# Kernel tuning notes

Measured on AMD Instinct MI355X. Metric: run time of the kernel, lower is better.

## Reference

```python
import jax, jax.numpy as jnp
import numpy as np

B, D_IN, D_CTX, UNITS, RANK = 4096, 2048, 512, 2048, 256


def setup_inputs() -> dict:
    key = jax.random.key(0)
    ks = jax.random.split(key, 6)
    scale_u = 1.0 / np.sqrt(D_IN)
    scale_w = 1.0 / np.sqrt(D_CTX)
    return {
        "inputs": jax.random.normal(ks[0], (B, D_IN), dtype=jnp.float32),
        "context": jax.random.normal(ks[1], (B, D_CTX), dtype=jnp.float32),
        "U": jax.random.normal(ks[2], (D_IN, RANK), dtype=jnp.float32) * scale_u,
        "S": jax.random.uniform(ks[3], (RANK,), dtype=jnp.float32) + 0.5,
        "V": jax.random.normal(ks[4], (UNITS, RANK), dtype=jnp.float32) * scale_u,
        "W": jax.random.normal(ks[5], (D_CTX, RANK), dtype=jnp.float32) * scale_w,
        "Bc": jnp.zeros((RANK,), dtype=jnp.float32),
        "bias": jnp.zeros((UNITS,), dtype=jnp.float32),
    }


def reference(inputs, context, U, S, V, W, Bc, bias):
    # h = context @ W + Bc ; chi = sigmoid(h) ; s[b,r] = S[r] * chi[b,r]
    chi = jax.nn.sigmoid(context @ W + Bc)           # [B, R]
    s = S * chi                                       # [B, R]
    # Original math: out[b,m] = sum_{n,r} x[b,n] U[n,r] s[b,r] V[m,r]
    # Reassociated (identical math, no [B,N,M] kernel): ((x @ U) * s) @ V^T
    proj = (inputs @ U) * s                           # [B, R]
    out = proj @ V.T + bias                           # [B, UNITS]
    return out  # activation is linear (None)
```

## Files before the change

kernel.cpp:

```cpp
#include <hip/hip_runtime.h>
#include <math.h>

namespace {

constexpr int Bdim  = 4096;
constexpr int D_IN  = 2048;
constexpr int D_CTX = 512;
constexpr int UNITS = 2048;
constexpr int RANK  = 256;
constexpr int SPLIT = 4;

typedef __bf16 bf16x8 __attribute__((ext_vector_type(8)));
typedef float  f32x4  __attribute__((ext_vector_type(4)));

__global__ __launch_bounds__(256) void k_prep(
    const float* __restrict__ U, const float* __restrict__ W,
    __bf16* __restrict__ Ut, __bf16* __restrict__ Wt) {
  const int job = blockIdx.y;
  const int t = threadIdx.x;
  const float* src = job ? W : U;
  __bf16* dst      = job ? Wt : Ut;
  const int K = job ? D_CTX : D_IN;
  const int tilesK = K / 64;
  const int tid = blockIdx.x;
  if (tid >= tilesK * 4) return;
  const int k0 = (tid % tilesK) * 64;
  const int n0 = (tid / tilesK) * 64;
  __shared__ __bf16 T[64][72];
  const int i  = t >> 4;
  const int j4 = (t & 15) * 4;
  for (int ii = i; ii < 64; ii += 16) {
    float4 v = *(const float4*)(src + (size_t)(k0 + ii) * RANK + n0 + j4);
    T[j4 + 0][ii] = (__bf16)v.x;
    T[j4 + 1][ii] = (__bf16)v.y;
    T[j4 + 2][ii] = (__bf16)v.z;
    T[j4 + 3][ii] = (__bf16)v.w;
  }
  __syncthreads();
  const int jj = t >> 3;
  const int c  = t & 7;
  for (int j2 = jj; j2 < 64; j2 += 32) {
    bf16x8 v = *(const bf16x8*)&T[j2][c * 8];
    *(bf16x8*)(dst + (size_t)(n0 + j2) * K + k0 + c * 8) = v;
  }
}

__global__ __launch_bounds__(256) void k_pg(
    const float* __restrict__ x,   const __bf16* __restrict__ Ut,
    const float* __restrict__ ctx, const __bf16* __restrict__ Wt,
    const float* __restrict__ S,   const float* __restrict__ Bc,
    __bf16* __restrict__ part, __bf16* __restrict__ s_out) {
  constexpr int BM = 64, BN = 128, BK = 64;
  __shared__ __align__(16) __bf16 As[2][BM * BK];
  __shared__ __align__(16) __bf16 Bs[2][BN * BK];
  const int t = threadIdx.x;
  const int y = blockIdx.y;
  const bool gate = (y < 2);
  const int nh    = gate ? y : ((y - 2) & 1);
  const int slice = (y - 2) >> 1;
  const int bm = blockIdx.x * BM;
  const int bn = nh * BN;
  const float*  A = gate ? ctx : x;
  const __bf16* B = gate ? Wt  : Ut;
  const int Kt   = gate ? D_CTX : D_IN;
  const int k_lo = gate ? 0 : slice * (D_IN / SPLIT);
  const int k_hi = gate ? D_CTX : k_lo + (D_IN / SPLIT);
  const int w = t >> 6, l = t & 63;
  const int wr0 = (w >> 1) * 32;
  const int wc0 = (w & 1) * 64;
  const int lrow = l & 15;
  const int lk   = l >> 4;
  f32x4 acc[2][4] = {};

  float4 a0_lo[2], a0_hi[2], a1_lo[2], a1_hi[2];
  bf16x8 b0[4], b1[4];

  auto LOADA = [&](float4 (&lo)[2], float4 (&hi)[2], int k0) {
#pragma unroll
    for (int ci = 0; ci < 2; ++ci) {
      const int c = t + ci * 256;
      const int row = c >> 3, kc = c & 7;
      const float* g = A + (size_t)(bm + row) * Kt + k0 + kc * 8;
      lo[ci] = *(const float4*)g;
      hi[ci] = *(const float4*)(g + 4);
    }
  };
  auto LOADB = [&](bf16x8 (&bb)[4], int k0) {
#pragma unroll
    for (int ci = 0; ci < 4; ++ci) {
      const int c = t + ci * 256;
      const int row = c >> 3, kc = c & 7;
      bb[ci] = *(const bf16x8*)(B + (size_t)(bn + row) * Kt + k0 + kc * 8);
    }
  };
  auto WRITEA = [&](char* dstAs, const float4 (&lo)[2], const float4 (&hi)[2]) {
#pragma unroll
    for (int ci = 0; ci < 2; ++ci) {
      const int c = t + ci * 256;
      const int row = c >> 3, kc = c & 7;
      bf16x8 v;
      v[0] = (__bf16)lo[ci].x; v[1] = (__bf16)lo[ci].y;
      v[2] = (__bf16)lo[ci].z; v[3] = (__bf16)lo[ci].w;
      v[4] = (__bf16)hi[ci].x; v[5] = (__bf16)hi[ci].y;
      v[6] = (__bf16)hi[ci].z; v[7] = (__bf16)hi[ci].w;
      *(bf16x8*)(dstAs + row * 128 + ((kc ^ (row & 7)) * 16)) = v;
    }
  };
  auto WRITEB = [&](char* dstBs, const bf16x8 (&bb)[4]) {
#pragma unroll
    for (int ci = 0; ci < 4; ++ci) {
      const int c = t + ci * 256;
      const int row = c >> 3, kc = c & 7;
      *(bf16x8*)(dstBs + row * 128 + ((kc ^ (row & 7)) * 16)) = bb[ci];
    }
  };
  auto MFMA_STEP = [&](const char* curAs, const char* curBs) {
#pragma unroll
    for (int kk = 0; kk < 2; ++kk) {
      bf16x8 af[2], bfr[4];
#pragma unroll
      for (int mf = 0; mf < 2; ++mf) {
        const int row = wr0 + mf * 16 + lrow;
        af[mf] = *(const bf16x8*)(curAs + row * 128 +
                                  (((kk * 4 + lk) ^ (row & 7)) * 16));
      }
#pragma unroll
      for (int nf = 0; nf < 4; ++nf) {
        const int row = wc0 + nf * 16 + lrow;
        bfr[nf] = *(const bf16x8*)(curBs + row * 128 +
                                   (((kk * 4 + lk) ^ (row & 7)) * 16));
      }
#pragma unroll
      for (int mf = 0; mf < 2; ++mf)
#pragma unroll
        for (int nf = 0; nf < 4; ++nf)
          acc[mf][nf] = __builtin_amdgcn_mfma_f32_16x16x32_bf16(
              af[mf], bfr[nf], acc[mf][nf], 0, 0, 0);
    }
  };

  LOADA(a0_lo, a0_hi, k_lo);
  LOADB(b0, k_lo);
  LOADA(a1_lo, a1_hi, k_lo + BK);
  LOADB(b1, k_lo + BK);
  for (int k0 = k_lo; k0 < k_hi; k0 += 2 * BK) {
    WRITEA((char*)As[0], a0_lo, a0_hi);
    WRITEB((char*)Bs[0], b0);
    __syncthreads();
    if (k0 + 2 * BK < k_hi) {
      LOADA(a0_lo, a0_hi, k0 + 2 * BK);
      LOADB(b0, k0 + 2 * BK);
    }
    MFMA_STEP((const char*)As[0], (const char*)Bs[0]);
    WRITEA((char*)As[1], a1_lo, a1_hi);
    WRITEB((char*)Bs[1], b1);
    __syncthreads();
    if (k0 + 3 * BK < k_hi) {
      LOADA(a1_lo, a1_hi, k0 + 3 * BK);
      LOADB(b1, k0 + 3 * BK);
    }
    MFMA_STEP((const char*)As[1], (const char*)Bs[1]);
  }

#pragma unroll
  for (int mf = 0; mf < 2; ++mf) {
#pragma unroll
    for (int nf = 0; nf < 4; ++nf) {
#pragma unroll
      for (int r = 0; r < 4; ++r) {
        const int m = bm + wr0 + mf * 16 + lk * 4 + r;
        const int n = bn + wc0 + nf * 16 + lrow;
        const float val = acc[mf][nf][r];
        if (gate) {
          const float h = val + Bc[n];
          s_out[(size_t)m * RANK + n] = (__bf16)(S[n] / (1.0f + __expf(-h)));
        } else {
          part[((size_t)slice * Bdim + m) * RANK + n] = (__bf16)val;
        }
      }
    }
  }
}

__global__ __launch_bounds__(256) void k_combine(
    const __bf16* __restrict__ part, const __bf16* __restrict__ s,
    __bf16* __restrict__ proj) {
  const size_t i8 = ((size_t)blockIdx.x * 256 + threadIdx.x) * 8;
  float sum[8] = {};
#pragma unroll
  for (int sl = 0; sl < SPLIT; ++sl) {
    bf16x8 v = *(const bf16x8*)(part + (size_t)sl * Bdim * RANK + i8);
#pragma unroll
    for (int i = 0; i < 8; ++i) sum[i] += (float)v[i];
  }
  bf16x8 sv = *(const bf16x8*)(s + i8);
  bf16x8 o;
#pragma unroll
  for (int i = 0; i < 8; ++i) o[i] = (__bf16)(sum[i] * (float)sv[i]);
  *(bf16x8*)(proj + i8) = o;
}

__global__ __launch_bounds__(256) void k_out(
    const __bf16* __restrict__ proj, const float* __restrict__ V,
    const float* __restrict__ bias, float* __restrict__ out) {
  constexpr int BM = 128, BN = 128, BK = 64;
  constexpr int Kt = RANK;
  __shared__ __align__(16) __bf16 As[BM * BK];
  __shared__ __align__(16) __bf16 Bs[BN * BK];
  const int t = threadIdx.x;
  const int lin = (int)(blockIdx.y * gridDim.x + blockIdx.x);
  const int swz = (lin & 7) * 64 + (lin >> 3);
  const int bm = (swz & 31) * BM;
  const int bn = (swz >> 5) * BN;
  const int w = t >> 6, l = t & 63;
  const int wr0 = (w >> 1) * 64;
  const int wc0 = (w & 1) * 64;
  const int lrow = l & 15;
  const int lk   = l >> 4;
  f32x4 acc[4][4] = {};

  bf16x8 a_bf[4];
  float4 b_lo[4], b_hi[4];

  auto LOADA = [&](int k0) {
#pragma unroll
    for (int ci = 0; ci < 4; ++ci) {
      const int c = t + ci * 256;
      const int row = c >> 3, kc = c & 7;
      a_bf[ci] = *(const bf16x8*)(proj + (size_t)(bm + row) * Kt + k0 + kc * 8);
    }
  };
  auto LOADB = [&](int k0) {
#pragma unroll
    for (int ci = 0; ci < 4; ++ci) {
      const int c = t + ci * 256;
      const int row = c >> 3, kc = c & 7;
      const float* g = V + (size_t)(bn + row) * Kt + k0 + kc * 8;
      b_lo[ci] = *(const float4*)g;
      b_hi[ci] = *(const float4*)(g + 4);
    }
  };
  auto WRITEA = [&]() {
#pragma unroll
    for (int ci = 0; ci < 4; ++ci) {
      const int c = t + ci * 256;
      const int row = c >> 3, kc = c & 7;
      *(bf16x8*)((char*)As + row * 128 + ((kc ^ (row & 7)) * 16)) = a_bf[ci];
    }
  };
  auto WRITEB = [&]() {
#pragma unroll
    for (int ci = 0; ci < 4; ++ci) {
      const int c = t + ci * 256;
      const int row = c >> 3, kc = c & 7;
      bf16x8 v;
      v[0] = (__bf16)b_lo[ci].x; v[1] = (__bf16)b_lo[ci].y;
      v[2] = (__bf16)b_lo[ci].z; v[3] = (__bf16)b_lo[ci].w;
      v[4] = (__bf16)b_hi[ci].x; v[5] = (__bf16)b_hi[ci].y;
      v[6] = (__bf16)b_hi[ci].z; v[7] = (__bf16)b_hi[ci].w;
      *(bf16x8*)((char*)Bs + row * 128 + ((kc ^ (row & 7)) * 16)) = v;
    }
  };

  LOADA(0);
  LOADB(0);
  for (int k0 = 0; k0 < Kt; k0 += BK) {
    WRITEA();
    WRITEB();
    __syncthreads();
    if (k0 + BK < Kt) {
      LOADA(k0 + BK);
      LOADB(k0 + BK);
    }
#pragma unroll
    for (int kk = 0; kk < 2; ++kk) {
      bf16x8 af[4], bfr[4];
#pragma unroll
      for (int mf = 0; mf < 4; ++mf) {
        const int row = wr0 + mf * 16 + lrow;
        af[mf] = *(const bf16x8*)((const char*)As + row * 128 +
                                  (((kk * 4 + lk) ^ (row & 7)) * 16));
      }
#pragma unroll
      for (int nf = 0; nf < 4; ++nf) {
        const int row = wc0 + nf * 16 + lrow;
        bfr[nf] = *(const bf16x8*)((const char*)Bs + row * 128 +
                                   (((kk * 4 + lk) ^ (row & 7)) * 16));
      }
#pragma unroll
      for (int mf = 0; mf < 4; ++mf)
#pragma unroll
        for (int nf = 0; nf < 4; ++nf)
          acc[mf][nf] = __builtin_amdgcn_mfma_f32_16x16x32_bf16(
              af[mf], bfr[nf], acc[mf][nf], 0, 0, 0);
    }
    __syncthreads();
  }

#pragma unroll
  for (int mf = 0; mf < 4; ++mf) {
#pragma unroll
    for (int nf = 0; nf < 4; ++nf) {
#pragma unroll
      for (int r = 0; r < 4; ++r) {
        const int m = bm + wr0 + mf * 16 + lk * 4 + r;
        const int n = bn + wc0 + nf * 16 + lrow;
        out[(size_t)m * UNITS + n] = acc[mf][nf][r] + bias[n];
      }
    }
  }
}

}

extern "C" void kernel_launch(void* const* d_in, const int* in_sizes, int n_in,
                              void* d_out, int out_size, void* d_ws, size_t ws_size,
                              hipStream_t stream) {
  const float* inputs  = (const float*)d_in[0];
  const float* context = (const float*)d_in[1];
  const float* U       = (const float*)d_in[2];
  const float* S       = (const float*)d_in[3];
  const float* V       = (const float*)d_in[4];
  const float* W       = (const float*)d_in[5];
  const float* Bc      = (const float*)d_in[6];
  const float* bias    = (const float*)d_in[7];
  float* out = (float*)d_out;

  char* ws = (char*)d_ws;
  __bf16* Ut   = (__bf16*)(ws);
  __bf16* Wt   = (__bf16*)(ws + 1048576);
  __bf16* proj = (__bf16*)(ws + 1310720);
  __bf16* sbuf = (__bf16*)(ws + 3407872);
  __bf16* part = (__bf16*)(ws + 5505024);

  k_prep<<<dim3(128, 2), 256, 0, stream>>>(U, W, Ut, Wt);

  k_pg<<<dim3(Bdim / 64, 2 * SPLIT + 2), 256, 0, stream>>>(
      inputs, Ut, context, Wt, S, Bc, part, sbuf);

  k_combine<<<dim3((Bdim * RANK) / (256 * 8)), 256, 0, stream>>>(part, sbuf, proj);

  k_out<<<dim3(Bdim / 128, UNITS / 128), 256, 0, stream>>>(proj, V, bias, out);
}
```

Before: 43.52 us.

## Load bf16 GEMM operands straight into LDS and double-buffer the output GEMM

In both MFMA GEMM kernels, the bf16 operand tiles (Ut/Wt in the projection kernel, proj in the output kernel) are now copied with global_load_lds. This moves data from global memory directly into LDS instead of staging it through registers and then issuing LDS stores, and it applies the XOR swizzle on the global-address side. The output kernel also switches from a single LDS buffer to two buffers, pipelining two k-steps so each iteration needs only one barrier. The intent is to cut VGPR pressure and LDS store instructions and to overlap loads with MFMA work. It relies on the barrier also covering completion of the asynchronous LDS writes, and it doubles the output kernel's LDS footprint.

```diff
diff --git a/kernel.cpp b/kernel.cpp
--- a/kernel.cpp
+++ b/kernel.cpp
@@ -12,6 +12,12 @@
 
 typedef __bf16 bf16x8 __attribute__((ext_vector_type(8)));
 typedef float  f32x4  __attribute__((ext_vector_type(4)));
+
+__device__ inline void gload16(const void* g, void* lds) {
+  __builtin_amdgcn_global_load_lds(
+      (const __attribute__((address_space(1))) void*)g,
+      (__attribute__((address_space(3))) void*)lds, 16, 0, 0);
+}
 
 __global__ __launch_bounds__(256) void k_prep(
     const float* __restrict__ U, const float* __restrict__ W,
@@ -73,7 +79,6 @@
   f32x4 acc[2][4] = {};
 
   float4 a0_lo[2], a0_hi[2], a1_lo[2], a1_hi[2];
-  bf16x8 b0[4], b1[4];
 
   auto LOADA = [&](float4 (&lo)[2], float4 (&hi)[2], int k0) {
 #pragma unroll
@@ -83,14 +88,6 @@
       const float* g = A + (size_t)(bm + row) * Kt + k0 + kc * 8;
       lo[ci] = *(const float4*)g;
       hi[ci] = *(const float4*)(g + 4);
-    }
-  };
-  auto LOADB = [&](bf16x8 (&bb)[4], int k0) {
-#pragma unroll
-    for (int ci = 0; ci < 4; ++ci) {
-      const int c = t + ci * 256;
-      const int row = c >> 3, kc = c & 7;
-      bb[ci] = *(const bf16x8*)(B + (size_t)(bn + row) * Kt + k0 + kc * 8);
     }
   };
   auto WRITEA = [&](char* dstAs, const float4 (&lo)[2], const float4 (&hi)[2]) {
@@ -106,12 +103,13 @@
       *(bf16x8*)(dstAs + row * 128 + ((kc ^ (row & 7)) * 16)) = v;
     }
   };
-  auto WRITEB = [&](char* dstBs, const bf16x8 (&bb)[4]) {
+  auto GLOADB = [&](char* dstBs, int k0) {
 #pragma unroll
     for (int ci = 0; ci < 4; ++ci) {
       const int c = t + ci * 256;
       const int row = c >> 3, kc = c & 7;
-      *(bf16x8*)(dstBs + row * 128 + ((kc ^ (row & 7)) * 16)) = bb[ci];
+      gload16(B + (size_t)(bn + row) * Kt + k0 + ((kc ^ (row & 7)) * 8),
+              dstBs + c * 16);
     }
   };
   auto MFMA_STEP = [&](const char* curAs, const char* curBs) {
@@ -139,26 +137,19 @@
     }
   };
 
+  GLOADB((char*)Bs[0], k_lo);
   LOADA(a0_lo, a0_hi, k_lo);
-  LOADB(b0, k_lo);
   LOADA(a1_lo, a1_hi, k_lo + BK);
-  LOADB(b1, k_lo + BK);
   for (int k0 = k_lo; k0 < k_hi; k0 += 2 * BK) {
     WRITEA((char*)As[0], a0_lo, a0_hi);
-    WRITEB((char*)Bs[0], b0);
     __syncthreads();
-    if (k0 + 2 * BK < k_hi) {
-      LOADA(a0_lo, a0_hi, k0 + 2 * BK);
-      LOADB(b0, k0 + 2 * BK);
-    }
+    if (k0 + BK < k_hi)     GLOADB((char*)Bs[1], k0 + BK);
+    if (k0 + 2 * BK < k_hi) LOADA(a0_lo, a0_hi, k0 + 2 * BK);
     MFMA_STEP((const char*)As[0], (const char*)Bs[0]);
     WRITEA((char*)As[1], a1_lo, a1_hi);
-    WRITEB((char*)Bs[1], b1);
     __syncthreads();
-    if (k0 + 3 * BK < k_hi) {
-      LOADA(a1_lo, a1_hi, k0 + 3 * BK);
-      LOADB(b1, k0 + 3 * BK);
-    }
+    if (k0 + 2 * BK < k_hi) GLOADB((char*)Bs[0], k0 + 2 * BK);
+    if (k0 + 3 * BK < k_hi) LOADA(a1_lo, a1_hi, k0 + 3 * BK);
     MFMA_STEP((const char*)As[1], (const char*)Bs[1]);
   }
 
@@ -205,8 +196,8 @@
     const float* __restrict__ bias, float* __restrict__ out) {
   constexpr int BM = 128, BN = 128, BK = 64;
   constexpr int Kt = RANK;
-  __shared__ __align__(16) __bf16 As[BM * BK];
-  __shared__ __align__(16) __bf16 Bs[BN * BK];
+  __shared__ __align__(16) __bf16 As[2][BM * BK];
+  __shared__ __align__(16) __bf16 Bs[2][BN * BK];
   const int t = threadIdx.x;
   const int lin = (int)(blockIdx.y * gridDim.x + blockIdx.x);
   const int swz = (lin & 7) * 64 + (lin >> 3);
@@ -219,72 +210,54 @@
   const int lk   = l >> 4;
   f32x4 acc[4][4] = {};
 
-  bf16x8 a_bf[4];
-  float4 b_lo[4], b_hi[4];
-
-  auto LOADA = [&](int k0) {
+  float4 b0_lo[4], b0_hi[4], b1_lo[4], b1_hi[4];
+
+  auto GLOADA = [&](char* dstAs, int k0) {
 #pragma unroll
     for (int ci = 0; ci < 4; ++ci) {
       const int c = t + ci * 256;
       const int row = c >> 3, kc = c & 7;
-      a_bf[ci] = *(const bf16x8*)(proj + (size_t)(bm + row) * Kt + k0 + kc * 8);
-    }
-  };
-  auto LOADB = [&](int k0) {
+      gload16(proj + (size_t)(bm + row) * Kt + k0 + ((kc ^ (row & 7)) * 8),
+              dstAs + c * 16);
+    }
+  };
+  auto LOADB = [&](float4 (&lo)[4], float4 (&hi)[4], int k0) {
 #pragma unroll
     for (int ci = 0; ci < 4; ++ci) {
       const int c = t + ci * 256;
       const int row = c >> 3, kc = c & 7;
       const float* g = V + (size_t)(bn + row) * Kt + k0 + kc * 8;
-      b_lo[ci] = *(const float4*)g;
-      b_hi[ci] = *(const float4*)(g + 4);
-    }
-  };
-  auto WRITEA = [&]() {
+      lo[ci] = *(const float4*)g;
+      hi[ci] = *(const float4*)(g + 4);
+    }
+  };
+  auto WRITEB = [&](char* dstBs, const float4 (&lo)[4], const float4 (&hi)[4]) {
 #pragma unroll
     for (int ci = 0; ci < 4; ++ci) {
       const int c = t + ci * 256;
       const int row = c >> 3, kc = c & 7;
-      *(bf16x8*)((char*)As + row * 128 + ((kc ^ (row & 7)) * 16)) = a_bf[ci];
-    }
-  };
-  auto WRITEB = [&]() {
-#pragma unroll
-    for (int ci = 0; ci < 4; ++ci) {
-      const int c = t + ci * 256;
-      const int row = c >> 3, kc = c & 7;
       bf16x8 v;
-      v[0] = (__bf16)b_lo[ci].x; v[1] = (__bf16)b_lo[ci].y;
-      v[2] = (__bf16)b_lo[ci].z; v[3] = (__bf16)b_lo[ci].w;
-      v[4] = (__bf16)b_hi[ci].x; v[5] = (__bf16)b_hi[ci].y;
-      v[6] = (__bf16)b_hi[ci].z; v[7] = (__bf16)b_hi[ci].w;
-      *(bf16x8*)((char*)Bs + row * 128 + ((kc ^ (row & 7)) * 16)) = v;
-    }
-  };
-
-  LOADA(0);
-  LOADB(0);
-  for (int k0 = 0; k0 < Kt; k0 += BK) {
-    WRITEA();
-    WRITEB();
-    __syncthreads();
-    if (k0 + BK < Kt) {
-      LOADA(k0 + BK);
-      LOADB(k0 + BK);
-    }
+      v[0] = (__bf16)lo[ci].x; v[1] = (__bf16)lo[ci].y;
+      v[2] = (__bf16)lo[ci].z; v[3] = (__bf16)lo[ci].w;
+      v[4] = (__bf16)hi[ci].x; v[5] = (__bf16)hi[ci].y;
+      v[6] = (__bf16)hi[ci].z; v[7] = (__bf16)hi[ci].w;
+      *(bf16x8*)(dstBs + row * 128 + ((kc ^ (row & 7)) * 16)) = v;
+    }
+  };
+  auto MFMA_STEP = [&](const char* curAs, const char* curBs) {
 #pragma unroll
     for (int kk = 0; kk < 2; ++kk) {
       bf16x8 af[4], bfr[4];
 #pragma unroll
       for (int mf = 0; mf < 4; ++mf) {
         const int row = wr0 + mf * 16 + lrow;
-        af[mf] = *(const bf16x8*)((const char*)As + row * 128 +
+        af[mf] = *(const bf16x8*)(curAs + row * 128 +
                                   (((kk * 4 + lk) ^ (row & 7)) * 16));
       }
 #pragma unroll
       for (int nf = 0; nf < 4; ++nf) {
         const int row = wc0 + nf * 16 + lrow;
-        bfr[nf] = *(const bf16x8*)((const char*)Bs + row * 128 +
+        bfr[nf] = *(const bf16x8*)(curBs + row * 128 +
                                    (((kk * 4 + lk) ^ (row & 7)) * 16));
       }
 #pragma unroll
@@ -294,7 +267,22 @@
           acc[mf][nf] = __builtin_amdgcn_mfma_f32_16x16x32_bf16(
               af[mf], bfr[nf], acc[mf][nf], 0, 0, 0);
     }
+  };
+
+  GLOADA((char*)As[0], 0);
+  LOADB(b0_lo, b0_hi, 0);
+  LOADB(b1_lo, b1_hi, BK);
+  for (int k0 = 0; k0 < Kt; k0 += 2 * BK) {
+    WRITEB((char*)Bs[0], b0_lo, b0_hi);
     __syncthreads();
+    if (k0 + BK < Kt)     GLOADA((char*)As[1], k0 + BK);
+    if (k0 + 2 * BK < Kt) LOADB(b0_lo, b0_hi, k0 + 2 * BK);
+    MFMA_STEP((const char*)As[0], (const char*)Bs[0]);
+    WRITEB((char*)Bs[1], b1_lo, b1_hi);
+    __syncthreads();
+    if (k0 + 2 * BK < Kt) GLOADA((char*)As[0], k0 + 2 * BK);
+    if (k0 + 3 * BK < Kt) LOADB(b1_lo, b1_hi, k0 + 3 * BK);
+    MFMA_STEP((const char*)As[1], (const char*)Bs[1]);
   }
 
 #pragma unroll
```

New measurement: 46.62 us. +7.1%, slower.

## Fuse split-K combine and gating into output GEMM A-tile staging

Applied to the files above, without the earlier changes.

Removes the separate combine kernel and has the output GEMM read the four split-K partials plus the gate directly while staging its A tile into LDS. It also double-buffers the shared-memory tiles so each k-step needs one barrier, and changes the tile swizzle so that consecutive blocks share M rows. This saves a launch and the write and reread of the proj buffer. In exchange, every N-tile block re-reads and re-sums the partials (16x redundant reads of part and s), and the A staging becomes synchronous global loads without prefetch.

```diff
diff --git a/kernel.cpp b/kernel.cpp
--- a/kernel.cpp
+++ b/kernel.cpp
@@ -182,36 +182,19 @@
   }
 }
 
-__global__ __launch_bounds__(256) void k_combine(
+__global__ __launch_bounds__(256) void k_out(
     const __bf16* __restrict__ part, const __bf16* __restrict__ s,
-    __bf16* __restrict__ proj) {
-  const size_t i8 = ((size_t)blockIdx.x * 256 + threadIdx.x) * 8;
-  float sum[8] = {};
-#pragma unroll
-  for (int sl = 0; sl < SPLIT; ++sl) {
-    bf16x8 v = *(const bf16x8*)(part + (size_t)sl * Bdim * RANK + i8);
-#pragma unroll
-    for (int i = 0; i < 8; ++i) sum[i] += (float)v[i];
-  }
-  bf16x8 sv = *(const bf16x8*)(s + i8);
-  bf16x8 o;
-#pragma unroll
-  for (int i = 0; i < 8; ++i) o[i] = (__bf16)(sum[i] * (float)sv[i]);
-  *(bf16x8*)(proj + i8) = o;
-}
-
-__global__ __launch_bounds__(256) void k_out(
-    const __bf16* __restrict__ proj, const float* __restrict__ V,
-    const float* __restrict__ bias, float* __restrict__ out) {
+    const float* __restrict__ V, const float* __restrict__ bias,
+    float* __restrict__ out) {
   constexpr int BM = 128, BN = 128, BK = 64;
   constexpr int Kt = RANK;
-  __shared__ __align__(16) __bf16 As[BM * BK];
-  __shared__ __align__(16) __bf16 Bs[BN * BK];
+  __shared__ __align__(16) __bf16 As[2][BM * BK];
+  __shared__ __align__(16) __bf16 Bs[2][BN * BK];
   const int t = threadIdx.x;
   const int lin = (int)(blockIdx.y * gridDim.x + blockIdx.x);
   const int swz = (lin & 7) * 64 + (lin >> 3);
-  const int bm = (swz & 31) * BM;
-  const int bn = (swz >> 5) * BN;
+  const int bm = (swz >> 4) * BM;
+  const int bn = (swz & 15) * BN;
   const int w = t >> 6, l = t & 63;
   const int wr0 = (w >> 1) * 64;
   const int wc0 = (w & 1) * 64;
@@ -219,17 +202,8 @@
   const int lk   = l >> 4;
   f32x4 acc[4][4] = {};
 
-  bf16x8 a_bf[4];
   float4 b_lo[4], b_hi[4];
 
-  auto LOADA = [&](int k0) {
-#pragma unroll
-    for (int ci = 0; ci < 4; ++ci) {
-      const int c = t + ci * 256;
-      const int row = c >> 3, kc = c & 7;
-      a_bf[ci] = *(const bf16x8*)(proj + (size_t)(bm + row) * Kt + k0 + kc * 8);
-    }
-  };
   auto LOADB = [&](int k0) {
 #pragma unroll
     for (int ci = 0; ci < 4; ++ci) {
@@ -240,15 +214,7 @@
       b_hi[ci] = *(const float4*)(g + 4);
     }
   };
-  auto WRITEA = [&]() {
-#pragma unroll
-    for (int ci = 0; ci < 4; ++ci) {
-      const int c = t + ci * 256;
-      const int row = c >> 3, kc = c & 7;
-      *(bf16x8*)((char*)As + row * 128 + ((kc ^ (row & 7)) * 16)) = a_bf[ci];
-    }
-  };
-  auto WRITEB = [&]() {
+  auto WRITEB = [&](char* dstBs) {
 #pragma unroll
     for (int ci = 0; ci < 4; ++ci) {
       const int c = t + ci * 256;
@@ -258,33 +224,43 @@
       v[2] = (__bf16)b_lo[ci].z; v[3] = (__bf16)b_lo[ci].w;
       v[4] = (__bf16)b_hi[ci].x; v[5] = (__bf16)b_hi[ci].y;
       v[6] = (__bf16)b_hi[ci].z; v[7] = (__bf16)b_hi[ci].w;
-      *(bf16x8*)((char*)Bs + row * 128 + ((kc ^ (row & 7)) * 16)) = v;
-    }
-  };
-
-  LOADA(0);
-  LOADB(0);
-  for (int k0 = 0; k0 < Kt; k0 += BK) {
-    WRITEA();
-    WRITEB();
-    __syncthreads();
-    if (k0 + BK < Kt) {
-      LOADA(k0 + BK);
-      LOADB(k0 + BK);
-    }
+      *(bf16x8*)(dstBs + row * 128 + ((kc ^ (row & 7)) * 16)) = v;
+    }
+  };
+  auto STAGEA = [&](char* dstAs, int k0) {
+#pragma unroll
+    for (int ci = 0; ci < 4; ++ci) {
+      const int c = t + ci * 256;
+      const int row = c >> 3, kc = c & 7;
+      const size_t off = (size_t)(bm + row) * RANK + k0 + kc * 8;
+      bf16x8 p0 = *(const bf16x8*)(part + off);
+      bf16x8 p1 = *(const bf16x8*)(part + (size_t)1 * Bdim * RANK + off);
+      bf16x8 p2 = *(const bf16x8*)(part + (size_t)2 * Bdim * RANK + off);
+      bf16x8 p3 = *(const bf16x8*)(part + (size_t)3 * Bdim * RANK + off);
+      bf16x8 sv = *(const bf16x8*)(s + off);
+      bf16x8 o;
+#pragma unroll
+      for (int i = 0; i < 8; ++i) {
+        const float sum = (float)p0[i] + (float)p1[i] + (float)p2[i] + (float)p3[i];
+        o[i] = (__bf16)(sum * (float)sv[i]);
+      }
+      *(bf16x8*)(dstAs + row * 128 + ((kc ^ (row & 7)) * 16)) = o;
+    }
+  };
+  auto MFMA_STEP = [&](const char* curAs, const char* curBs) {
 #pragma unroll
     for (int kk = 0; kk < 2; ++kk) {
       bf16x8 af[4], bfr[4];
 #pragma unroll
       for (int mf = 0; mf < 4; ++mf) {
         const int row = wr0 + mf * 16 + lrow;
-        af[mf] = *(const bf16x8*)((const char*)As + row * 128 +
+        af[mf] = *(const bf16x8*)(curAs + row * 128 +
                                   (((kk * 4 + lk) ^ (row & 7)) * 16));
       }
 #pragma unroll
       for (int nf = 0; nf < 4; ++nf) {
         const int row = wc0 + nf * 16 + lrow;
-        bfr[nf] = *(const bf16x8*)((const char*)Bs + row * 128 +
+        bfr[nf] = *(const bf16x8*)(curBs + row * 128 +
                                    (((kk * 4 + lk) ^ (row & 7)) * 16));
       }
 #pragma unroll
@@ -294,7 +270,20 @@
           acc[mf][nf] = __builtin_amdgcn_mfma_f32_16x16x32_bf16(
               af[mf], bfr[nf], acc[mf][nf], 0, 0, 0);
     }
+  };
+
+  LOADB(0);
+  for (int k0 = 0; k0 < Kt; k0 += 2 * BK) {
+    STAGEA((char*)As[0], k0);
+    WRITEB((char*)Bs[0]);
     __syncthreads();
+    if (k0 + BK < Kt) LOADB(k0 + BK);
+    MFMA_STEP((const char*)As[0], (const char*)Bs[0]);
+    STAGEA((char*)As[1], k0 + BK);
+    WRITEB((char*)Bs[1]);
+    __syncthreads();
+    if (k0 + 2 * BK < Kt) LOADB(k0 + 2 * BK);
+    MFMA_STEP((const char*)As[1], (const char*)Bs[1]);
   }
 
 #pragma unroll
@@ -329,16 +318,14 @@
   char* ws = (char*)d_ws;
   __bf16* Ut   = (__bf16*)(ws);
   __bf16* Wt   = (__bf16*)(ws + 1048576);
-  __bf16* proj = (__bf16*)(ws + 1310720);
-  __bf16* sbuf = (__bf16*)(ws + 3407872);
-  __bf16* part = (__bf16*)(ws + 5505024);
+  __bf16* sbuf = (__bf16*)(ws + 1310720);
+  __bf16* part = (__bf16*)(ws + 3407872);
 
   k_prep<<<dim3(128, 2), 256, 0, stream>>>(U, W, Ut, Wt);
 
   k_pg<<<dim3(Bdim / 64, 2 * SPLIT + 2), 256, 0, stream>>>(
       inputs, Ut, context, Wt, S, Bc, part, sbuf);
 
-  k_combine<<<dim3((Bdim * RANK) / (256 * 8)), 256, 0, stream>>>(part, sbuf, proj);
-
-  k_out<<<dim3(Bdim / 128, UNITS / 128), 256, 0, stream>>>(proj, V, bias, out);
-}
+  k_out<<<dim3(Bdim / 128, UNITS / 128), 256, 0, stream>>>(
+      part, sbuf, V, bias, out);
+}
```

New measurement: 44.12 us. About the same (+1.4%).
